# Optimization experiments

Hardware: AMD Instinct MI355X
Metric: run time of the kernel (lower is better)

## Reference

```python
import jax, jax.numpy as jnp
import numpy as np

N_ROWS = 4096
SIG_LEN = 16384
FILT_LEN = 8


def setup_inputs() -> dict:
    key = jax.random.key(0)
    k_in, k_sc = jax.random.split(key)
    inp = jax.random.normal(k_in, (N_ROWS, SIG_LEN), dtype=jnp.float32)
    scaling = jax.random.normal(k_sc, (FILT_LEN,), dtype=jnp.float32)
    return {"input": inp, "scaling": scaling}


def compute_wavelet(scaling):
    # g_k = h_{M-k-1}, then negate odd-indexed taps (quadrature mirror filter)
    g = jnp.flip(scaling, axis=-1)
    signs = jnp.where(jnp.arange(scaling.shape[-1]) % 2 == 1, -1.0, 1.0).astype(scaling.dtype)
    return g * signs


def reference(input, scaling):
    m = input.shape[-1]
    wavelet = compute_wavelet(scaling)
    # circular FFT convolution (filter zero-padded to n=m), as in the torch code.
    ra = jnp.fft.rfft(input)  # [n, m//2+1] complex — computed once, reused for both filters
    details = jnp.fft.irfft(ra * jnp.fft.rfft(wavelet, n=m), n=m)
    approximation = jnp.fft.irfft(ra * jnp.fft.rfft(scaling, n=m), n=m)
    # stride-2 downsample (DWT decimation)
    return details[:, ::2], approximation[:, ::2]
```

## Files before the change

### kernel.cpp

```cpp
#include <hip/hip_runtime.h>


#define N_ROWS   4096
#define SIG_LEN  16384
#define HALF_LEN (SIG_LEN / 2)
#define THREADS_PER_ROW (HALF_LEN / 8)

__global__ __launch_bounds__(256) void dwt_fwd_kernel(
    const float* __restrict__ input,
    const float* __restrict__ scaling,
    float* __restrict__ details,
    float* __restrict__ approx)
{
    const int tid = blockIdx.x * blockDim.x + threadIdx.x;
    const int row = tid >> 10;
    const int seg = tid & 1023;
    if (row >= N_ROWS) return;

    float h[8], w[8];
#pragma unroll
    for (int k = 0; k < 8; ++k) h[k] = scaling[k];
#pragma unroll
    for (int k = 0; k < 8; ++k) w[k] = h[7 - k] * ((k & 1) ? -1.0f : 1.0f);

    const int i0 = seg << 4;
    const float* rowp = input + (size_t)row * SIG_LEN;

    float x[24];

    {
        const int hbase = (i0 == 0) ? (SIG_LEN - 8) : (i0 - 8);
        const float4 a = *reinterpret_cast<const float4*>(rowp + hbase);
        const float4 b = *reinterpret_cast<const float4*>(rowp + hbase + 4);
        x[0] = a.x; x[1] = a.y; x[2] = a.z; x[3] = a.w;
        x[4] = b.x; x[5] = b.y; x[6] = b.z; x[7] = b.w;
    }
#pragma unroll
    for (int q = 0; q < 4; ++q) {
        const float4 v = *reinterpret_cast<const float4*>(rowp + i0 + 4 * q);
        x[8 + 4 * q + 0] = v.x;
        x[8 + 4 * q + 1] = v.y;
        x[8 + 4 * q + 2] = v.z;
        x[8 + 4 * q + 3] = v.w;
    }

    float det[8], app[8];
#pragma unroll
    for (int j = 0; j < 8; ++j) {
        const int base = 8 + 2 * j;
        float d = 0.0f, a = 0.0f;
#pragma unroll
        for (int k = 0; k < 8; ++k) {
            const float xi = x[base - k];
            d = fmaf(w[k], xi, d);
            a = fmaf(h[k], xi, a);
        }
        det[j] = d;
        app[j] = a;
    }

    const size_t obase = (size_t)row * HALF_LEN + (size_t)(seg << 3);
    float4* dp = reinterpret_cast<float4*>(details + obase);
    float4* ap = reinterpret_cast<float4*>(approx + obase);
    dp[0] = make_float4(det[0], det[1], det[2], det[3]);
    dp[1] = make_float4(det[4], det[5], det[6], det[7]);
    ap[0] = make_float4(app[0], app[1], app[2], app[3]);
    ap[1] = make_float4(app[4], app[5], app[6], app[7]);
}

extern "C" void kernel_launch(void* const* d_in, const int* in_sizes, int n_in,
                              void* d_out, int out_size, void* d_ws, size_t ws_size,
                              hipStream_t stream) {
    const float* input   = (const float*)d_in[0];
    const float* scaling = (const float*)d_in[1];
    float* details = (float*)d_out;
    float* approx  = (float*)d_out + (size_t)N_ROWS * HALF_LEN;

    const int total_threads = N_ROWS * THREADS_PER_ROW;
    const int block = 256;
    const int grid  = total_threads / block;
    dwt_fwd_kernel<<<grid, block, 0, stream>>>(input, scaling, details, approx);
}
```

Measured before the change: 101.3 us.

## Shrink per-thread work to 4 inputs with coalesced loads and nontemporal stores

```diff
diff --git a/kernel.cpp b/kernel.cpp
--- a/kernel.cpp
+++ b/kernel.cpp
@@ -4,7 +4,10 @@
 #define N_ROWS   4096
 #define SIG_LEN  16384
 #define HALF_LEN (SIG_LEN / 2)
-#define THREADS_PER_ROW (HALF_LEN / 8)
+#define CHUNKS_PER_ROW (SIG_LEN / 4)
+
+typedef float f32x2 __attribute__((ext_vector_type(2)));
+typedef float f32x4 __attribute__((ext_vector_type(4)));
 
 __global__ __launch_bounds__(256) void dwt_fwd_kernel(
     const float* __restrict__ input,
@@ -12,10 +15,10 @@
     float* __restrict__ details,
     float* __restrict__ approx)
 {
-    const int tid = blockIdx.x * blockDim.x + threadIdx.x;
-    const int row = tid >> 10;
-    const int seg = tid & 1023;
-    if (row >= N_ROWS) return;
+    const int c   = blockIdx.x * blockDim.x + threadIdx.x;
+    const int row = c >> 12;
+    const int cl  = c & (CHUNKS_PER_ROW - 1);
+    const int p   = cl << 2;
 
     float h[8], w[8];
 #pragma unroll
@@ -23,49 +26,36 @@
 #pragma unroll
     for (int k = 0; k < 8; ++k) w[k] = h[7 - k] * ((k & 1) ? -1.0f : 1.0f);
 
-    const int i0 = seg << 4;
     const float* rowp = input + (size_t)row * SIG_LEN;
 
-    float x[24];
+    int a0 = p - 8; if (a0 < 0) a0 += SIG_LEN;
+    int a1 = p - 4; if (a1 < 0) a1 += SIG_LEN;
 
-    {
-        const int hbase = (i0 == 0) ? (SIG_LEN - 8) : (i0 - 8);
-        const float4 a = *reinterpret_cast<const float4*>(rowp + hbase);
-        const float4 b = *reinterpret_cast<const float4*>(rowp + hbase + 4);
-        x[0] = a.x; x[1] = a.y; x[2] = a.z; x[3] = a.w;
-        x[4] = b.x; x[5] = b.y; x[6] = b.z; x[7] = b.w;
-    }
+    const f32x4 hA = *reinterpret_cast<const f32x4*>(rowp + a0);
+    const f32x4 hB = *reinterpret_cast<const f32x4*>(rowp + a1);
+    const f32x4 m  = *reinterpret_cast<const f32x4*>(rowp + p);
+
+    float y[12];
+    y[0] = hA.x; y[1] = hA.y; y[2]  = hA.z; y[3]  = hA.w;
+    y[4] = hB.x; y[5] = hB.y; y[6]  = hB.z; y[7]  = hB.w;
+    y[8] = m.x;  y[9] = m.y;  y[10] = m.z;  y[11] = m.w;
+
+    float d0 = 0.f, a0f = 0.f, d1 = 0.f, a1f = 0.f;
 #pragma unroll
-    for (int q = 0; q < 4; ++q) {
-        const float4 v = *reinterpret_cast<const float4*>(rowp + i0 + 4 * q);
-        x[8 + 4 * q + 0] = v.x;
-        x[8 + 4 * q + 1] = v.y;
-        x[8 + 4 * q + 2] = v.z;
-        x[8 + 4 * q + 3] = v.w;
+    for (int k = 0; k < 8; ++k) {
+        const float x0 = y[8 - k];
+        const float x1 = y[10 - k];
+        d0  = fmaf(w[k], x0, d0);
+        a0f = fmaf(h[k], x0, a0f);
+        d1  = fmaf(w[k], x1, d1);
+        a1f = fmaf(h[k], x1, a1f);
     }
 
-    float det[8], app[8];
-#pragma unroll
-    for (int j = 0; j < 8; ++j) {
-        const int base = 8 + 2 * j;
-        float d = 0.0f, a = 0.0f;
-#pragma unroll
-        for (int k = 0; k < 8; ++k) {
-            const float xi = x[base - k];
-            d = fmaf(w[k], xi, d);
-            a = fmaf(h[k], xi, a);
-        }
-        det[j] = d;
-        app[j] = a;
-    }
-
-    const size_t obase = (size_t)row * HALF_LEN + (size_t)(seg << 3);
-    float4* dp = reinterpret_cast<float4*>(details + obase);
-    float4* ap = reinterpret_cast<float4*>(approx + obase);
-    dp[0] = make_float4(det[0], det[1], det[2], det[3]);
-    dp[1] = make_float4(det[4], det[5], det[6], det[7]);
-    ap[0] = make_float4(app[0], app[1], app[2], app[3]);
-    ap[1] = make_float4(app[4], app[5], app[6], app[7]);
+    const size_t obase = (size_t)row * HALF_LEN + (size_t)(cl << 1);
+    f32x2 dv; dv.x = d0;  dv.y = d1;
+    f32x2 av; av.x = a0f; av.y = a1f;
+    __builtin_nontemporal_store(dv, reinterpret_cast<f32x2*>(details + obase));
+    __builtin_nontemporal_store(av, reinterpret_cast<f32x2*>(approx + obase));
 }
 
 extern "C" void kernel_launch(void* const* d_in, const int* in_sizes, int n_in,
@@ -76,7 +66,7 @@
     float* details = (float*)d_out;
     float* approx  = (float*)d_out + (size_t)N_ROWS * HALF_LEN;
 
-    const int total_threads = N_ROWS * THREADS_PER_ROW;
+    const int total_threads = N_ROWS * CHUNKS_PER_ROW;
     const int block = 256;
     const int grid  = total_threads / block;
     dwt_fwd_kernel<<<grid, block, 0, stream>>>(input, scaling, details, approx);
```

After: 81.77 us. 19.3% less time.
